# Performance work log

Hardware: AMD Instinct MI355X
Metric: run time of the kernel (lower is better)

Reference implementation:

```python
import jax, jax.numpy as jnp
import numpy as np

N_NODES = 100      # fixed: actor_fc expects 6000 = 100 * 60
IN_C    = 65536    # chev_conv_state_dim
OUT_C   = 60
K       = 3        # Chebyshev order
ACTION  = 100
N_EDGES = 1600


def setup_inputs() -> dict:
    key = jax.random.key(0)
    ks = jax.random.split(key, 20)
    s = 0.02  # small init scale
    f32 = jnp.float32
    return {
        "substrate_features": jax.random.normal(ks[0], (N_NODES, IN_C), f32),
        "substrate_edge_index": jax.random.randint(ks[1], (2, N_EDGES), 0, N_NODES),
        "vnr_features": jax.random.uniform(ks[2], (1, 3), f32),
        # ChebConv params: weight [K, IN_C, OUT_C], bias [OUT_C]
        "actor_cheb_w": (jax.random.normal(ks[3], (K, IN_C, OUT_C), f32) * s),
        "actor_cheb_b": jnp.zeros((OUT_C,), f32),
        "critic_cheb_w": (jax.random.normal(ks[4], (K, IN_C, OUT_C), f32) * s),
        "critic_cheb_b": jnp.zeros((OUT_C,), f32),
        # three Linear(1,60) per head, stacked: w [3, 60], b [3, 60]
        "actor_vnr_w": jax.random.normal(ks[5], (3, OUT_C), f32) * s,
        "actor_vnr_b": jnp.zeros((3, OUT_C), f32),
        "critic_vnr_w": jax.random.normal(ks[6], (3, OUT_C), f32) * s,
        "critic_vnr_b": jnp.zeros((3, OUT_C), f32),
        # heads
        "actor_fc_w": jax.random.normal(ks[7], (N_NODES * OUT_C, ACTION), f32) * s,
        "actor_fc_b": jnp.zeros((ACTION,), f32),
        "critic_fc_w": jax.random.normal(ks[8], (N_NODES * OUT_C, 1), f32) * s,
        "critic_fc_b": jnp.zeros((1,), f32),
    }


def _cheb_conv(x, src, dst, W, b):
    """PyG ChebConv with sym normalization, lambda_max=2 => L_hat = -D^-1/2 A D^-1/2.
    Z0 = x, Z1 = L_hat x, Z2 = 2 L_hat Z1 - Z0; out = sum_k Zk @ W[k] + b."""
    n = x.shape[0]
    ones = jnp.ones(src.shape[0], x.dtype)
    deg = jax.ops.segment_sum(ones, src, num_segments=n)
    dinv = jnp.where(deg > 0, jax.lax.rsqrt(jnp.maximum(deg, 1.0)), 0.0)
    w_norm = -dinv[src] * dinv[dst]  # [E]

    def lhat(z):  # sparse propagate: gather src rows, scale, scatter-add at dst
        return jax.ops.segment_sum(w_norm[:, None] * z[src], dst, num_segments=n)

    z0 = x
    z1 = lhat(z0)
    z2 = 2.0 * lhat(z1) - z0
    return z0 @ W[0] + z1 @ W[1] + z2 @ W[2] + b


def _vnr_sum(v, w, b):
    # sum of three Linear(1,60) outputs on scalars v[0], v[1], v[2] -> [60]
    return (v[:, None] * w + b).sum(axis=0)


def reference(substrate_features, substrate_edge_index, vnr_features,
              actor_cheb_w, actor_cheb_b, critic_cheb_w, critic_cheb_b,
              actor_vnr_w, actor_vnr_b, critic_vnr_w, critic_vnr_b,
              actor_fc_w, actor_fc_b, critic_fc_w, critic_fc_b):
    src, dst = substrate_edge_index[0], substrate_edge_index[1]
    v = vnr_features[0]  # [3]

    emb_a = jnp.tanh(_cheb_conv(substrate_features, src, dst, actor_cheb_w, actor_cheb_b))
    emb_a = emb_a + _vnr_sum(v, actor_vnr_w, actor_vnr_b)  # broadcast [N,60] + [60]
    flat_a = emb_a.reshape(1, -1)  # [1, 6000]
    logits = flat_a @ actor_fc_w + actor_fc_b  # [1, ACTION]

    emb_c = jnp.tanh(_cheb_conv(substrate_features, src, dst, critic_cheb_w, critic_cheb_b))
    emb_c = emb_c + _vnr_sum(v, critic_vnr_w, critic_vnr_b)
    flat_c = emb_c.reshape(1, -1)
    values = flat_c @ critic_fc_w + critic_fc_b  # [1, 1]

    return logits, values
```

## Files before the change

### kernel.cpp

```cpp
#include <hip/hip_runtime.h>
#include <math.h>

#define KDIM    65536
#define NNODES  100
#define OUTC    60
#define YW      64
#define YSLAB   (NNODES*YW)

#define BK5     64
#define ITERS5  8
#define SLAB5   (BK5*ITERS5)
#define NKC5    (KDIM/SLAB5)
#define CHUNK   256
#define NKC     256
#define STEPS   (CHUNK/32)

#define WS_Y    10048
#define WS_E    48448
#define XB_OFF_BYTES   245760ull
#define XB_BYTES       (100ull*65536ull*2ull)
#define WS_NEED_BYTES  (XB_OFF_BYTES + XB_BYTES)

typedef short bf16x8 __attribute__((ext_vector_type(8)));
typedef float f32x4  __attribute__((ext_vector_type(4)));
typedef unsigned short ushort8 __attribute__((ext_vector_type(8)));

__device__ inline unsigned short f2bf(float f) {
    union { float f; unsigned u; } x; x.f = f;
    unsigned r = x.u + 0x7FFFu + ((x.u >> 16) & 1u);
    return (unsigned short)(r >> 16);
}

__global__ __launch_bounds__(256) void k_cvt_x(const float* __restrict__ x,
                                               ushort8* __restrict__ xb,
                                               float* __restrict__ Y,
                                               float* __restrict__ out) {
    int g = blockIdx.x * 256 + threadIdx.x;
    if (g < 9600) ((f32x4*)Y)[g] = (f32x4){};
    if (g < 101)  out[g] = 0.f;
    for (int i = g; i < 819200; i += 204800) {
        const float4 lo = ((const float4*)x)[2 * i];
        const float4 hi = ((const float4*)x)[2 * i + 1];
        ushort8 o;
        o[0] = f2bf(lo.x); o[1] = f2bf(lo.y); o[2] = f2bf(lo.z); o[3] = f2bf(lo.w);
        o[4] = f2bf(hi.x); o[5] = f2bf(hi.y); o[6] = f2bf(hi.z); o[7] = f2bf(hi.w);
        xb[i] = o;
    }
}

__global__ __launch_bounds__(256) void k_gemm8(const unsigned short* __restrict__ xb,
                                               const float* __restrict__ wa,
                                               const float* __restrict__ wc,
                                               float* __restrict__ Y) {
    __shared__ unsigned short Ab[2][14 * 512];
    __shared__ unsigned short padlds[512];
    const int b    = blockIdx.x;
    const int lo8  = b & 7, q = b >> 3;
    const int hk   = q % 6;
    const int kc   = lo8 + 8 * (q / 6);
    const int wave = threadIdx.x >> 6;
    const int lane = threadIdx.x & 63;
    const int n16  = lane & 15;
    const int quad = lane >> 4;
    const int c0   = wave * 16;
    const int cidx = min(c0 + n16, OUTC - 1);
    const int kb0  = kc * SLAB5;

    const float* Wg = (hk < 3 ? wa : wc) + (size_t)(hk % 3) * ((size_t)KDIM * OUTC);

    auto DMA = [&](int buf, int kb) {
#pragma unroll
        for (int j5 = 0; j5 < 4; ++j5) {
            int j = wave + j5 * 4;
            int chunk = j * 64 + lane;
            int m  = chunk >> 3;
            int cc = (chunk & 7) ^ (m & 7);
            const unsigned short* src =
                xb + (size_t)min(m, NNODES - 1) * KDIM + kb + cc * 8;
            void* dst = (j < 14) ? (void*)&Ab[buf][j * 512] : (void*)padlds;
            __builtin_amdgcn_global_load_lds(
                (const __attribute__((address_space(1))) void*)src,
                (__attribute__((address_space(3))) void*)dst, 16, 0, 0);
        }
    };

    float breg[2][16];
    auto LOADB = [&](int pb, int kb) {
        const float* base = Wg + (size_t)(kb + quad * 8) * OUTC + cidx;
#pragma unroll
        for (int s = 0; s < 2; ++s)
#pragma unroll
            for (int j = 0; j < 8; ++j)
                breg[pb][s * 8 + j] = base[(s * 32 + j) * OUTC];
    };

    DMA(0, kb0);
    LOADB(0, kb0);
    f32x4 acc[7] = {};

#pragma unroll
    for (int it = 0; it < ITERS5; ++it) {
        if (it + 1 < ITERS5) {
            DMA((it + 1) & 1, kb0 + (it + 1) * BK5);
            LOADB((it + 1) & 1, kb0 + (it + 1) * BK5);
            asm volatile("s_waitcnt vmcnt(20)" ::: "memory");
        } else {
            asm volatile("s_waitcnt vmcnt(0)" ::: "memory");
        }
        __builtin_amdgcn_s_barrier();
        const unsigned short* A = Ab[it & 1];
#pragma unroll
        for (int s = 0; s < 2; ++s) {
            bf16x8 bfr;
#pragma unroll
            for (int j = 0; j < 8; ++j)
                bfr[j] = (short)f2bf(breg[it & 1][s * 8 + j]);
            int ch = (s * 4 + quad) ^ (n16 & 7);
#pragma unroll
            for (int t = 0; t < 7; ++t) {
                bf16x8 afr = *(const bf16x8*)(A + (t * 16 + n16) * BK5 + ch * 8);
                acc[t] = __builtin_amdgcn_mfma_f32_16x16x32_bf16(afr, bfr, acc[t], 0, 0, 0);
            }
        }
        __builtin_amdgcn_s_barrier();
    }

    float* Yb = Y + hk * YSLAB;
#pragma unroll
    for (int t = 0; t < 7; ++t)
#pragma unroll
        for (int r = 0; r < 4; ++r) {
            int row = t * 16 + quad * 4 + r;
            if (row < NNODES)
                atomicAdd(&Yb[row * YW + c0 + n16], acc[t][r]);
        }
}

__global__ __launch_bounds__(256, 2) void k_gemm_f32(const float* __restrict__ x,
                                                     const float* __restrict__ wa,
                                                     const float* __restrict__ wc,
                                                     float* __restrict__ Y) {
    const int hk   = blockIdx.x;
    const int kc   = blockIdx.y;
    const int wave = threadIdx.x >> 6;
    const int lane = threadIdx.x & 63;
    const int n16  = lane & 15;
    const int quad = lane >> 4;
    const float* W = (hk < 3 ? wa : wc) + (size_t)(hk % 3) * ((size_t)KDIM * OUTC);
    const int c0   = wave * 16;
    const int cidx = min(c0 + n16, OUTC - 1);
    const int kb0  = kc * CHUNK + quad * 8;
    const float* ap[7];
#pragma unroll
    for (int t = 0; t < 7; ++t)
        ap[t] = x + (size_t)min(n16 + 16 * t, NNODES - 1) * KDIM + kb0;
    const float* bp = W + (size_t)kb0 * OUTC + cidx;
    f32x4 acc[7] = {};
#pragma unroll 2
    for (int s = 0; s < STEPS; ++s) {
        bf16x8 bfr;
        const float* qq = bp + (size_t)s * 32 * OUTC;
#pragma unroll
        for (int j = 0; j < 8; ++j) bfr[j] = (short)f2bf(qq[j * OUTC]);
#pragma unroll
        for (int t = 0; t < 7; ++t) {
            const float* p = ap[t] + s * 32;
            float4 lo = *(const float4*)p;
            float4 hi = *(const float4*)(p + 4);
            bf16x8 afr;
            afr[0] = (short)f2bf(lo.x); afr[1] = (short)f2bf(lo.y);
            afr[2] = (short)f2bf(lo.z); afr[3] = (short)f2bf(lo.w);
            afr[4] = (short)f2bf(hi.x); afr[5] = (short)f2bf(hi.y);
            afr[6] = (short)f2bf(hi.z); afr[7] = (short)f2bf(hi.w);
            acc[t] = __builtin_amdgcn_mfma_f32_16x16x32_bf16(afr, bfr, acc[t], 0, 0, 0);
        }
    }
    float* Yb = Y + hk * YSLAB;
#pragma unroll
    for (int t = 0; t < 7; ++t)
#pragma unroll
        for (int r = 0; r < 4; ++r) {
            int row = t * 16 + quad * 4 + r;
            if (row < NNODES)
                atomicAdd(&Yb[row * YW + c0 + n16], acc[t][r]);
        }
}

__global__ __launch_bounds__(128) void k_embh(const int* __restrict__ ei,
                                              const float* __restrict__ Y,
                                              const float* __restrict__ vnr,
                                              const float* __restrict__ avw,
                                              const float* __restrict__ avb,
                                              const float* __restrict__ cvw,
                                              const float* __restrict__ cvb,
                                              const float* __restrict__ acb,
                                              const float* __restrict__ ccb,
                                              const float* __restrict__ afcb,
                                              const float* __restrict__ cfcb,
                                              const float* __restrict__ afw,
                                              const float* __restrict__ cfw,
                                              float* __restrict__ out) {
    __shared__ float Sp[NNODES * 101];
    __shared__ float y0[NNODES], y1[NNODES], y2[NNODES], t2[NNODES];
    __shared__ float e[NNODES];
    __shared__ int   deg[NNODES];
    __shared__ float dinv[NNODES];
    const int b = blockIdx.x, head = b / OUTC, c = b % OUTC;
    const int t = threadIdx.x;
    const int* src = ei;
    const int* dst = ei + 1600;

    for (int i = t; i < NNODES * 101; i += 128) Sp[i] = 0.f;
    if (t < NNODES) deg[t] = 0;
    __syncthreads();
    for (int ed = t; ed < 1600; ed += 128) atomicAdd(&deg[src[ed]], 1);
    __syncthreads();
    if (t < NNODES) { int d = deg[t]; dinv[t] = (d > 0) ? rsqrtf((float)d) : 0.f; }
    __syncthreads();
    for (int ed = t; ed < 1600; ed += 128) {
        int s = src[ed], d = dst[ed];
        atomicAdd(&Sp[d * 101 + s], -dinv[s] * dinv[d]);
    }
    const float* Yh = Y + (size_t)head * 3 * YSLAB;
    if (t < NNODES) {
        y0[t] = Yh[t * YW + c];
        y1[t] = Yh[YSLAB + t * YW + c];
        y2[t] = Yh[2 * YSLAB + t * YW + c];
    }
    __syncthreads();

    float z1 = 0.f, s2 = 0.f;
    if (t < NNODES) {
        const float* sr = Sp + t * 101;
        for (int m = 0; m < NNODES; ++m) { z1 += sr[m] * y1[m]; s2 += sr[m] * y2[m]; }
        t2[t] = s2;
    }
    __syncthreads();
    float ev = 0.f;
    if (t < NNODES) {
        const float* sr = Sp + t * 101;
        float t3 = 0.f;
        for (int m = 0; m < NNODES; ++m) t3 += sr[m] * t2[m];
        const float* cb = head ? ccb : acb;
        const float* vw = head ? cvw : avw;
        const float* vb = head ? cvb : avb;
        float u  = y0[t] + z1 + 2.f * t3 - y2[t] + cb[c];
        float vs = vnr[0] * vw[c]        + vb[c]
                 + vnr[1] * vw[OUTC + c] + vb[OUTC + c]
                 + vnr[2] * vw[2*OUTC+c] + vb[2*OUTC+c];
        ev = tanhf(u) + vs;
        e[t] = ev;
    }
    __syncthreads();

    if (head == 0) {
        if (t < NNODES) {
            float s = (c == 0) ? afcb[t] : 0.f;
            const float* wrow = afw + (size_t)c * 100 + t;
#pragma unroll 4
            for (int n = 0; n < NNODES; ++n) s += e[n] * wrow[(size_t)n * 6000];
            atomicAdd(&out[t], s);
        }
    } else {
        float p = (t < NNODES) ? ev * cfw[t * OUTC + c] : 0.f;
#pragma unroll
        for (int off = 32; off > 0; off >>= 1) p += __shfl_down(p, off, 64);
        __shared__ float wsum[2];
        if ((t & 63) == 0) wsum[t >> 6] = p;
        __syncthreads();
        if (t == 0) atomicAdd(&out[100], wsum[0] + wsum[1] + (c == 0 ? cfcb[0] : 0.f));
    }
}

extern "C" void kernel_launch(void* const* d_in, const int* in_sizes, int n_in,
                              void* d_out, int out_size, void* d_ws, size_t ws_size,
                              hipStream_t stream) {
    const float* x    = (const float*)d_in[0];
    const int*   ei   = (const int*)  d_in[1];
    const float* vnr  = (const float*)d_in[2];
    const float* wa   = (const float*)d_in[3];
    const float* acb  = (const float*)d_in[4];
    const float* wc   = (const float*)d_in[5];
    const float* ccb  = (const float*)d_in[6];
    const float* avw  = (const float*)d_in[7];
    const float* avb  = (const float*)d_in[8];
    const float* cvw  = (const float*)d_in[9];
    const float* cvb  = (const float*)d_in[10];
    const float* afw  = (const float*)d_in[11];
    const float* afcb = (const float*)d_in[12];
    const float* cfw  = (const float*)d_in[13];
    const float* cfcb = (const float*)d_in[14];

    float* ws = (float*)d_ws;
    float* Y  = ws + WS_Y;
    float* out = (float*)d_out;

    if (ws_size >= WS_NEED_BYTES) {
        unsigned short* xb = (unsigned short*)((char*)d_ws + XB_OFF_BYTES);
        k_cvt_x<<<800, 256, 0, stream>>>(x, (ushort8*)xb, Y, out);
        k_gemm8<<<768, 256, 0, stream>>>(xb, wa, wc, Y);
    } else {
        hipMemsetAsync((char*)d_ws + WS_Y * 4, 0, (WS_E - WS_Y) * 4, stream);
        hipMemsetAsync(d_out, 0, 101 * sizeof(float), stream);
        k_gemm_f32<<<dim3(6, NKC), 256, 0, stream>>>(x, wa, wc, Y);
    }

    k_embh<<<120, 128, 0, stream>>>(ei, Y, vnr, avw, avb, cvw, cvb,
                                    acb, ccb, afcb, cfcb, afw, cfw, out);
}
```

Measured before the change: 205.5 us.

## Share X tile across all six weight slabs in one 384-thread block

Replaces the per-(head,k) GEMM blocks with a single block per 256-wide K chunk in which six waves each own one of the six weight matrices. The bf16 X tile for the chunk is loaded into LDS once and reused by all six heads, removing the redundant X reads across six separate blocks. Each wave now covers all 60 output columns with a 4x7 accumulator set, and the double-buffered pipelining is replaced by one upfront load followed by a barrier. This raises register pressure, removes the overlap of loads with compute, and leaves 256 blocks in the grid.

```diff
diff --git a/kernel.cpp b/kernel.cpp
--- a/kernel.cpp
+++ b/kernel.cpp
@@ -7,10 +7,10 @@
 #define YW      64
 #define YSLAB   (NNODES*YW)
 
-#define BK5     64
-#define ITERS5  8
-#define SLAB5   (BK5*ITERS5)
-#define NKC5    (KDIM/SLAB5)
+#define BKA     64
+#define NSUB    4
+#define SLABA   (BKA*NSUB)
+#define NKCA    (KDIM/SLABA)
 #define CHUNK   256
 #define NKC     256
 #define STEPS   (CHUNK/32)
@@ -48,92 +48,77 @@
     }
 }
 
-__global__ __launch_bounds__(256) void k_gemm8(const unsigned short* __restrict__ xb,
-                                               const float* __restrict__ wa,
-                                               const float* __restrict__ wc,
-                                               float* __restrict__ Y) {
-    __shared__ unsigned short Ab[2][14 * 512];
-    __shared__ unsigned short padlds[512];
-    const int b    = blockIdx.x;
-    const int lo8  = b & 7, q = b >> 3;
-    const int hk   = q % 6;
-    const int kc   = lo8 + 8 * (q / 6);
+__global__ __launch_bounds__(384) void k_gemm10(const unsigned short* __restrict__ xb,
+                                                const float* __restrict__ wa,
+                                                const float* __restrict__ wc,
+                                                float* __restrict__ Y) {
+    __shared__ unsigned short Ab[NSUB][14 * 512];
+    const int kc   = blockIdx.x;
     const int wave = threadIdx.x >> 6;
     const int lane = threadIdx.x & 63;
     const int n16  = lane & 15;
     const int quad = lane >> 4;
-    const int c0   = wave * 16;
-    const int cidx = min(c0 + n16, OUTC - 1);
-    const int kb0  = kc * SLAB5;
-
-    const float* Wg = (hk < 3 ? wa : wc) + (size_t)(hk % 3) * ((size_t)KDIM * OUTC);
-
-    auto DMA = [&](int buf, int kb) {
-#pragma unroll
-        for (int j5 = 0; j5 < 4; ++j5) {
-            int j = wave + j5 * 4;
-            int chunk = j * 64 + lane;
-            int m  = chunk >> 3;
-            int cc = (chunk & 7) ^ (m & 7);
-            const unsigned short* src =
-                xb + (size_t)min(m, NNODES - 1) * KDIM + kb + cc * 8;
-            void* dst = (j < 14) ? (void*)&Ab[buf][j * 512] : (void*)padlds;
-            __builtin_amdgcn_global_load_lds(
-                (const __attribute__((address_space(1))) void*)src,
-                (__attribute__((address_space(3))) void*)dst, 16, 0, 0);
-        }
-    };
-
-    float breg[2][16];
-    auto LOADB = [&](int pb, int kb) {
-        const float* base = Wg + (size_t)(kb + quad * 8) * OUTC + cidx;
-#pragma unroll
-        for (int s = 0; s < 2; ++s)
-#pragma unroll
-            for (int j = 0; j < 8; ++j)
-                breg[pb][s * 8 + j] = base[(s * 32 + j) * OUTC];
-    };
-
-    DMA(0, kb0);
-    LOADB(0, kb0);
-    f32x4 acc[7] = {};
-
-#pragma unroll
-    for (int it = 0; it < ITERS5; ++it) {
-        if (it + 1 < ITERS5) {
-            DMA((it + 1) & 1, kb0 + (it + 1) * BK5);
-            LOADB((it + 1) & 1, kb0 + (it + 1) * BK5);
-            asm volatile("s_waitcnt vmcnt(20)" ::: "memory");
-        } else {
-            asm volatile("s_waitcnt vmcnt(0)" ::: "memory");
-        }
-        __builtin_amdgcn_s_barrier();
-        const unsigned short* A = Ab[it & 1];
+    const int kb0  = kc * SLABA;
+
+    const float* Wg = (wave < 3 ? wa : wc) + (size_t)(wave % 3) * ((size_t)KDIM * OUTC);
+
+    for (int jj = wave; jj < 56; jj += 6) {
+        int sub = jj / 14, j = jj % 14;
+        int chunk = j * 64 + lane;
+        int m  = chunk >> 3;
+        int cc = (chunk & 7) ^ (m & 7);
+        const unsigned short* src =
+            xb + (size_t)min(m, NNODES - 1) * KDIM + kb0 + sub * BKA + cc * 8;
+        __builtin_amdgcn_global_load_lds(
+            (const __attribute__((address_space(1))) void*)src,
+            (__attribute__((address_space(3))) void*)&Ab[sub][j * 512], 16, 0, 0);
+    }
+    __syncthreads();
+
+    f32x4 acc[4][7] = {};
+
+#pragma unroll
+    for (int sub = 0; sub < NSUB; ++sub) {
 #pragma unroll
         for (int s = 0; s < 2; ++s) {
-            bf16x8 bfr;
-#pragma unroll
-            for (int j = 0; j < 8; ++j)
-                bfr[j] = (short)f2bf(breg[it & 1][s * 8 + j]);
-            int ch = (s * 4 + quad) ^ (n16 & 7);
-#pragma unroll
-            for (int t = 0; t < 7; ++t) {
-                bf16x8 afr = *(const bf16x8*)(A + (t * 16 + n16) * BK5 + ch * 8);
-                acc[t] = __builtin_amdgcn_mfma_f32_16x16x32_bf16(afr, bfr, acc[t], 0, 0, 0);
+            float bv[4][8];
+            const int k0 = kb0 + sub * BKA + s * 32 + quad * 8;
+#pragma unroll
+            for (int ng = 0; ng < 4; ++ng) {
+                const int cidx = min(ng * 16 + n16, OUTC - 1);
+                const float* bp = Wg + (size_t)k0 * OUTC + cidx;
+#pragma unroll
+                for (int j = 0; j < 8; ++j) bv[ng][j] = bp[j * OUTC];
             }
-        }
-        __builtin_amdgcn_s_barrier();
-    }
-
-    float* Yb = Y + hk * YSLAB;
-#pragma unroll
-    for (int t = 0; t < 7; ++t)
-#pragma unroll
-        for (int r = 0; r < 4; ++r) {
-            int row = t * 16 + quad * 4 + r;
-            if (row < NNODES)
-                atomicAdd(&Yb[row * YW + c0 + n16], acc[t][r]);
-        }
+            const int ch = (s * 4 + quad) ^ (n16 & 7);
+            bf16x8 afr[7];
+#pragma unroll
+            for (int t = 0; t < 7; ++t)
+                afr[t] = *(const bf16x8*)(&Ab[sub][(t * 16 + n16) * BKA + ch * 8]);
+#pragma unroll
+            for (int ng = 0; ng < 4; ++ng) {
+                bf16x8 bfr;
+#pragma unroll
+                for (int j = 0; j < 8; ++j) bfr[j] = (short)f2bf(bv[ng][j]);
+#pragma unroll
+                for (int t = 0; t < 7; ++t)
+                    acc[ng][t] = __builtin_amdgcn_mfma_f32_16x16x32_bf16(
+                        afr[t], bfr, acc[ng][t], 0, 0, 0);
+            }
+        }
+    }
+
+    float* Yb = Y + wave * YSLAB;
+#pragma unroll
+    for (int ng = 0; ng < 4; ++ng)
+#pragma unroll
+        for (int t = 0; t < 7; ++t)
+#pragma unroll
+            for (int r = 0; r < 4; ++r) {
+                int row = t * 16 + quad * 4 + r;
+                if (row < NNODES)
+                    atomicAdd(&Yb[row * YW + ng * 16 + n16], acc[ng][t][r]);
+            }
 }
 
 __global__ __launch_bounds__(256, 2) void k_gemm_f32(const float* __restrict__ x,
@@ -298,7 +283,7 @@
     if (ws_size >= WS_NEED_BYTES) {
         unsigned short* xb = (unsigned short*)((char*)d_ws + XB_OFF_BYTES);
         k_cvt_x<<<800, 256, 0, stream>>>(x, (ushort8*)xb, Y, out);
-        k_gemm8<<<768, 256, 0, stream>>>(xb, wa, wc, Y);
+        k_gemm10<<<NKCA, 384, 0, stream>>>(xb, wa, wc, Y);
     } else {
         hipMemsetAsync((char*)d_ws + WS_Y * 4, 0, (WS_E - WS_Y) * 4, stream);
         hipMemsetAsync(d_out, 0, 101 * sizeof(float), stream);
```

After: 249.4 us. +21.4%, slower.

## Pre-transpose weights to bf16, triple-buffer GEMM, fuse epilogue via cooperative grid sync

Applied to the files above, without the earlier changes.

A new prep kernel converts both heads' Chebyshev weights to bf16 each call. It uses an LDS-staged transpose into a packed layout, so the GEMM can load each B fragment with one 16-byte vector load instead of 16 strided scalar fp32 loads plus per-element conversion. The GEMM moves to three-stage buffering with twice the K-slab per block (384 blocks). It is fused with the graph-propagation/head epilogue through a cooperative grid sync, with the old two-kernel path kept as a fallback. The trade-off is an extra full write and re-read of the bf16 weight copy, plus the cost of a grid-wide barrier.

```diff
diff --git a/kernel.cpp b/kernel.cpp
--- a/kernel.cpp
+++ b/kernel.cpp
@@ -1,4 +1,5 @@
 #include <hip/hip_runtime.h>
+#include <hip/hip_cooperative_groups.h>
 #include <math.h>
 
 #define KDIM    65536
@@ -7,10 +8,9 @@
 #define YW      64
 #define YSLAB   (NNODES*YW)
 
-#define BK5     64
-#define ITERS5  8
-#define SLAB5   (BK5*ITERS5)
-#define NKC5    (KDIM/SLAB5)
+#define BK      64
+#define ITERS   16
+#define SLAB    (BK*ITERS)
 #define CHUNK   256
 #define NKC     256
 #define STEPS   (CHUNK/32)
@@ -19,7 +19,10 @@
 #define WS_E    48448
 #define XB_OFF_BYTES   245760ull
 #define XB_BYTES       (100ull*65536ull*2ull)
-#define WS_NEED_BYTES  (XB_OFF_BYTES + XB_BYTES)
+#define WT_OFF_BYTES   (XB_OFF_BYTES + XB_BYTES)
+#define WT_HK_USH      (8192ull*60ull*8ull)
+#define WT_BYTES       (6ull*WT_HK_USH*2ull)
+#define WS_NEED_BYTES  (WT_OFF_BYTES + WT_BYTES)
 
 typedef short bf16x8 __attribute__((ext_vector_type(8)));
 typedef float f32x4  __attribute__((ext_vector_type(4)));
@@ -31,14 +34,19 @@
     return (unsigned short)(r >> 16);
 }
 
-__global__ __launch_bounds__(256) void k_cvt_x(const float* __restrict__ x,
-                                               ushort8* __restrict__ xb,
-                                               float* __restrict__ Y,
-                                               float* __restrict__ out) {
-    int g = blockIdx.x * 256 + threadIdx.x;
+__global__ __launch_bounds__(256) void k_prep(const float* __restrict__ x,
+                                              const float* __restrict__ wa,
+                                              const float* __restrict__ wc,
+                                              ushort8* __restrict__ xb,
+                                              unsigned short* __restrict__ wt,
+                                              float* __restrict__ Y,
+                                              float* __restrict__ out) {
+    __shared__ float tile[15360];
+    const int t  = threadIdx.x;
+    const int g  = blockIdx.x * 256 + t;
     if (g < 9600) ((f32x4*)Y)[g] = (f32x4){};
     if (g < 101)  out[g] = 0.f;
-    for (int i = g; i < 819200; i += 204800) {
+    for (int i = g; i < 819200; i += 393216) {
         const float4 lo = ((const float4*)x)[2 * i];
         const float4 hi = ((const float4*)x)[2 * i + 1];
         ushort8 o;
@@ -46,14 +54,210 @@
         o[4] = f2bf(hi.x); o[5] = f2bf(hi.y); o[6] = f2bf(hi.z); o[7] = f2bf(hi.w);
         xb[i] = o;
     }
-}
-
-__global__ __launch_bounds__(256) void k_gemm8(const unsigned short* __restrict__ xb,
-                                               const float* __restrict__ wa,
-                                               const float* __restrict__ wc,
-                                               float* __restrict__ Y) {
-    __shared__ unsigned short Ab[2][14 * 512];
-    __shared__ unsigned short padlds[512];
+    const int hk   = blockIdx.x >> 8;
+    const int ws_  = blockIdx.x & 255;
+    const int kb   = ws_ * 256;
+    const float* Wg = (hk < 3 ? wa : wc) + (size_t)(hk % 3) * ((size_t)KDIM * OUTC);
+    const float4* src4 = (const float4*)(Wg + (size_t)kb * OUTC);
+#pragma unroll
+    for (int i = 0; i < 15; ++i)
+        ((float4*)tile)[t + i * 256] = src4[t + i * 256];
+    __syncthreads();
+    ushort8* dst = (ushort8*)(wt + (size_t)hk * WT_HK_USH) + (size_t)(ws_ * 32) * 60;
+#pragma unroll
+    for (int i = 0; i < 8; ++i) {
+        int idx2 = t + i * 256;
+        if (idx2 < 1920) {
+            int pp = idx2 / 60, c = idx2 - pp * 60;
+            ushort8 o;
+#pragma unroll
+            for (int j = 0; j < 8; ++j) o[j] = f2bf(tile[(pp * 8 + j) * 60 + c]);
+            dst[idx2] = o;
+        }
+    }
+}
+
+union SMem {
+    struct { unsigned short Ab[3][14 * 512]; unsigned short pad[512]; } g;
+    struct { float Sp[NNODES * 101]; float y0[NNODES], y1[NNODES], y2[NNODES],
+             t2[NNODES], e[NNODES]; int deg[NNODES]; float dinv[NNODES];
+             float wsum[4]; } h;
+};
+
+__global__ __launch_bounds__(256) void k_main(const unsigned short* __restrict__ xb,
+                                              const unsigned short* __restrict__ wt,
+                                              float* __restrict__ Y,
+                                              const int* __restrict__ ei,
+                                              const float* __restrict__ vnr,
+                                              const float* __restrict__ avw,
+                                              const float* __restrict__ avb,
+                                              const float* __restrict__ cvw,
+                                              const float* __restrict__ cvb,
+                                              const float* __restrict__ acb,
+                                              const float* __restrict__ ccb,
+                                              const float* __restrict__ afcb,
+                                              const float* __restrict__ cfcb,
+                                              const float* __restrict__ afw,
+                                              const float* __restrict__ cfw,
+                                              float* __restrict__ out) {
+    __shared__ SMem sm;
+    {
+        const int b    = blockIdx.x;
+        const int lo8  = b & 7, q = b >> 3;
+        const int hk   = q % 6;
+        const int kc   = lo8 + 8 * (q / 6);
+        const int wave = threadIdx.x >> 6;
+        const int lane = threadIdx.x & 63;
+        const int n16  = lane & 15;
+        const int quad = lane >> 4;
+        const int c0   = wave * 16;
+        const int cidx = min(c0 + n16, OUTC - 1);
+        const int kb0  = kc * SLAB;
+
+        const unsigned short* wth = wt + (size_t)hk * WT_HK_USH;
+
+        auto DMA = [&](int buf, int kb) {
+#pragma unroll
+            for (int j5 = 0; j5 < 4; ++j5) {
+                int j = wave + j5 * 4;
+                int chunk = j * 64 + lane;
+                int m  = chunk >> 3;
+                int cc = (chunk & 7) ^ (m & 7);
+                const unsigned short* src =
+                    xb + (size_t)min(m, NNODES - 1) * KDIM + kb + cc * 8;
+                void* dst = (j < 14) ? (void*)&sm.g.Ab[buf][j * 512] : (void*)sm.g.pad;
+                __builtin_amdgcn_global_load_lds(
+                    (const __attribute__((address_space(1))) void*)src,
+                    (__attribute__((address_space(3))) void*)dst, 16, 0, 0);
+            }
+        };
+        bf16x8 breg[3][2];
+        auto LOADB = [&](int pb, int kb) {
+            const int pbase = kb >> 3;
+#pragma unroll
+            for (int s = 0; s < 2; ++s) {
+                size_t idx = (size_t)(pbase + s * 4 + quad) * 60 + cidx;
+                breg[pb][s] = *(const bf16x8*)(wth + idx * 8);
+            }
+        };
+
+        DMA(0, kb0);           LOADB(0, kb0);
+        DMA(1, kb0 + BK);      LOADB(1, kb0 + BK);
+        f32x4 acc[7] = {};
+
+#pragma unroll
+        for (int it = 0; it < ITERS; ++it) {
+            if (it + 2 < ITERS) {
+                DMA((it + 2) % 3, kb0 + (it + 2) * BK);
+                LOADB((it + 2) % 3, kb0 + (it + 2) * BK);
+                asm volatile("s_waitcnt vmcnt(12)" ::: "memory");
+            } else if (it + 2 == ITERS) {
+                asm volatile("s_waitcnt vmcnt(6)" ::: "memory");
+            } else {
+                asm volatile("s_waitcnt vmcnt(0)" ::: "memory");
+            }
+            __builtin_amdgcn_s_barrier();
+            const unsigned short* A = sm.g.Ab[it % 3];
+#pragma unroll
+            for (int s = 0; s < 2; ++s) {
+                bf16x8 bfr = breg[it % 3][s];
+                int ch = (s * 4 + quad) ^ (n16 & 7);
+#pragma unroll
+                for (int t = 0; t < 7; ++t) {
+                    bf16x8 afr = *(const bf16x8*)(A + (t * 16 + n16) * BK + ch * 8);
+                    acc[t] = __builtin_amdgcn_mfma_f32_16x16x32_bf16(afr, bfr, acc[t], 0, 0, 0);
+                }
+            }
+            __builtin_amdgcn_s_barrier();
+        }
+
+        float* Yb = Y + hk * YSLAB;
+#pragma unroll
+        for (int t = 0; t < 7; ++t)
+#pragma unroll
+            for (int r = 0; r < 4; ++r) {
+                int row = t * 16 + quad * 4 + r;
+                if (row < NNODES)
+                    atomicAdd(&Yb[row * YW + c0 + n16], acc[t][r]);
+            }
+    }
+
+    cooperative_groups::this_grid().sync();
+
+    const int b = blockIdx.x;
+    if (b >= 120) return;
+    const int head = b / OUTC, c = b % OUTC;
+    const int t = threadIdx.x;
+    const int* src = ei;
+    const int* dst = ei + 1600;
+
+    for (int i = t; i < NNODES * 101; i += 256) sm.h.Sp[i] = 0.f;
+    if (t < NNODES) sm.h.deg[t] = 0;
+    __syncthreads();
+    for (int ed = t; ed < 1600; ed += 256) atomicAdd(&sm.h.deg[src[ed]], 1);
+    __syncthreads();
+    if (t < NNODES) { int d = sm.h.deg[t]; sm.h.dinv[t] = (d > 0) ? rsqrtf((float)d) : 0.f; }
+    __syncthreads();
+    for (int ed = t; ed < 1600; ed += 256) {
+        int s = src[ed], d = dst[ed];
+        atomicAdd(&sm.h.Sp[d * 101 + s], -sm.h.dinv[s] * sm.h.dinv[d]);
+    }
+    float* Yh = Y + (size_t)head * 3 * YSLAB;
+    if (t < NNODES) {
+        sm.h.y0[t] = atomicAdd(&Yh[t * YW + c], 0.f);
+        sm.h.y1[t] = atomicAdd(&Yh[YSLAB + t * YW + c], 0.f);
+        sm.h.y2[t] = atomicAdd(&Yh[2 * YSLAB + t * YW + c], 0.f);
+    }
+    __syncthreads();
+
+    float z1 = 0.f, s2 = 0.f;
+    if (t < NNODES) {
+        const float* sr = sm.h.Sp + t * 101;
+        for (int m = 0; m < NNODES; ++m) { z1 += sr[m] * sm.h.y1[m]; s2 += sr[m] * sm.h.y2[m]; }
+        sm.h.t2[t] = s2;
+    }
+    __syncthreads();
+    float ev = 0.f;
+    if (t < NNODES) {
+        const float* sr = sm.h.Sp + t * 101;
+        float t3 = 0.f;
+        for (int m = 0; m < NNODES; ++m) t3 += sr[m] * sm.h.t2[m];
+        const float* cb = head ? ccb : acb;
+        const float* vw = head ? cvw : avw;
+        const float* vb = head ? cvb : avb;
+        float u  = sm.h.y0[t] + z1 + 2.f * t3 - sm.h.y2[t] + cb[c];
+        float vs = vnr[0] * vw[c]        + vb[c]
+                 + vnr[1] * vw[OUTC + c] + vb[OUTC + c]
+                 + vnr[2] * vw[2*OUTC+c] + vb[2*OUTC+c];
+        ev = tanhf(u) + vs;
+        sm.h.e[t] = ev;
+    }
+    __syncthreads();
+
+    if (head == 0) {
+        if (t < NNODES) {
+            float s = (c == 0) ? afcb[t] : 0.f;
+            const float* wrow = afw + (size_t)c * 100 + t;
+#pragma unroll 4
+            for (int n = 0; n < NNODES; ++n) s += sm.h.e[n] * wrow[(size_t)n * 6000];
+            atomicAdd(&out[t], s);
+        }
+    } else {
+        float p = (t < NNODES) ? ev * cfw[t * OUTC + c] : 0.f;
+#pragma unroll
+        for (int off = 32; off > 0; off >>= 1) p += __shfl_down(p, off, 64);
+        if ((t & 63) == 0) sm.h.wsum[t >> 6] = p;
+        __syncthreads();
+        if (t == 0) atomicAdd(&out[100],
+            sm.h.wsum[0] + sm.h.wsum[1] + sm.h.wsum[2] + sm.h.wsum[3] +
+            (c == 0 ? cfcb[0] : 0.f));
+    }
+}
+
+__global__ __launch_bounds__(256) void k_gemm_nc(const unsigned short* __restrict__ xb,
+                                                 const unsigned short* __restrict__ wt,
+                                                 float* __restrict__ Y) {
+    __shared__ SMem sm;
     const int b    = blockIdx.x;
     const int lo8  = b & 7, q = b >> 3;
     const int hk   = q % 6;
@@ -64,9 +268,8 @@
     const int quad = lane >> 4;
     const int c0   = wave * 16;
     const int cidx = min(c0 + n16, OUTC - 1);
-    const int kb0  = kc * SLAB5;
-
-    const float* Wg = (hk < 3 ? wa : wc) + (size_t)(hk % 3) * ((size_t)KDIM * OUTC);
+    const int kb0  = kc * SLAB;
+    const unsigned short* wth = wt + (size_t)hk * WT_HK_USH;
 
     auto DMA = [&](int buf, int kb) {
 #pragma unroll
@@ -77,48 +280,46 @@
             int cc = (chunk & 7) ^ (m & 7);
             const unsigned short* src =
                 xb + (size_t)min(m, NNODES - 1) * KDIM + kb + cc * 8;
-            void* dst = (j < 14) ? (void*)&Ab[buf][j * 512] : (void*)padlds;
+            void* dst = (j < 14) ? (void*)&sm.g.Ab[buf][j * 512] : (void*)sm.g.pad;
             __builtin_amdgcn_global_load_lds(
                 (const __attribute__((address_space(1))) void*)src,
                 (__attribute__((address_space(3))) void*)dst, 16, 0, 0);
         }
     };
-
-    float breg[2][16];
+    bf16x8 breg[3][2];
     auto LOADB = [&](int pb, int kb) {
-        const float* base = Wg + (size_t)(kb + quad * 8) * OUTC + cidx;
-#pragma unroll
-        for (int s = 0; s < 2; ++s)
-#pragma unroll
-            for (int j = 0; j < 8; ++j)
-                breg[pb][s * 8 + j] = base[(s * 32 + j) * OUTC];
+        const int pbase = kb >> 3;
+#pragma unroll
+        for (int s = 0; s < 2; ++s) {
+            size_t idx = (size_t)(pbase + s * 4 + quad) * 60 + cidx;
+            breg[pb][s] = *(const bf16x8*)(wth + idx * 8);
+        }
     };
 
-    DMA(0, kb0);
-    LOADB(0, kb0);
+    DMA(0, kb0);           LOADB(0, kb0);
+    DMA(1, kb0 + BK);      LOADB(1, kb0 + BK);
     f32x4 acc[7] = {};
 
 #pragma unroll
-    for (int it = 0; it < ITERS5; ++it) {
-        if (it + 1 < ITERS5) {
-            DMA((it + 1) & 1, kb0 + (it + 1) * BK5);
-            LOADB((it + 1) & 1, kb0 + (it + 1) * BK5);
-            asm volatile("s_waitcnt vmcnt(20)" ::: "memory");
+    for (int it = 0; it < ITERS; ++it) {
+        if (it + 2 < ITERS) {
+            DMA((it + 2) % 3, kb0 + (it + 2) * BK);
+            LOADB((it + 2) % 3, kb0 + (it + 2) * BK);
+            asm volatile("s_waitcnt vmcnt(12)" ::: "memory");
+        } else if (it + 2 == ITERS) {
+            asm volatile("s_waitcnt vmcnt(6)" ::: "memory");
         } else {
             asm volatile("s_waitcnt vmcnt(0)" ::: "memory");
         }
         __builtin_amdgcn_s_barrier();
-        const unsigned short* A = Ab[it & 1];
+        const unsigned short* A = sm.g.Ab[it % 3];
 #pragma unroll
         for (int s = 0; s < 2; ++s) {
-            bf16x8 bfr;
-#pragma unroll
-            for (int j = 0; j < 8; ++j)
-                bfr[j] = (short)f2bf(breg[it & 1][s * 8 + j]);
+            bf16x8 bfr = breg[it % 3][s];
             int ch = (s * 4 + quad) ^ (n16 & 7);
 #pragma unroll
             for (int t = 0; t < 7; ++t) {
-                bf16x8 afr = *(const bf16x8*)(A + (t * 16 + n16) * BK5 + ch * 8);
+                bf16x8 afr = *(const bf16x8*)(A + (t * 16 + n16) * BK + ch * 8);
                 acc[t] = __builtin_amdgcn_mfma_f32_16x16x32_bf16(afr, bfr, acc[t], 0, 0, 0);
             }
         }
@@ -134,6 +335,88 @@
             if (row < NNODES)
                 atomicAdd(&Yb[row * YW + c0 + n16], acc[t][r]);
         }
+}
+
+__global__ __launch_bounds__(128) void k_embh_fb(const int* __restrict__ ei,
+                                                 const float* __restrict__ Y,
+                                                 const float* __restrict__ vnr,
+                                                 const float* __restrict__ avw,
+                                                 const float* __restrict__ avb,
+                                                 const float* __restrict__ cvw,
+                                                 const float* __restrict__ cvb,
+                                                 const float* __restrict__ acb,
+                                                 const float* __restrict__ ccb,
+                                                 const float* __restrict__ afcb,
+                                                 const float* __restrict__ cfcb,
+                                                 const float* __restrict__ afw,
+                                                 const float* __restrict__ cfw,
+                                                 float* __restrict__ out) {
+    __shared__ float Sp[NNODES * 101];
+    __shared__ float y0[NNODES], y1[NNODES], y2[NNODES], t2[NNODES], e[NNODES];
+    __shared__ int   deg[NNODES];
+    __shared__ float dinv[NNODES];
+    const int b = blockIdx.x, head = b / OUTC, c = b % OUTC;
+    const int t = threadIdx.x;
+    const int* src = ei;
+    const int* dst = ei + 1600;
+    for (int i = t; i < NNODES * 101; i += 128) Sp[i] = 0.f;
+    if (t < NNODES) deg[t] = 0;
+    __syncthreads();
+    for (int ed = t; ed < 1600; ed += 128) atomicAdd(&deg[src[ed]], 1);
+    __syncthreads();
+    if (t < NNODES) { int d = deg[t]; dinv[t] = (d > 0) ? rsqrtf((float)d) : 0.f; }
+    __syncthreads();
+    for (int ed = t; ed < 1600; ed += 128) {
+        int s = src[ed], d = dst[ed];
+        atomicAdd(&Sp[d * 101 + s], -dinv[s] * dinv[d]);
+    }
+    const float* Yh = Y + (size_t)head * 3 * YSLAB;
+    if (t < NNODES) {
+        y0[t] = Yh[t * YW + c];
+        y1[t] = Yh[YSLAB + t * YW + c];
+        y2[t] = Yh[2 * YSLAB + t * YW + c];
+    }
+    __syncthreads();
+    float z1 = 0.f, s2 = 0.f;
+    if (t < NNODES) {
+        const float* sr = Sp + t * 101;
+        for (int m = 0; m < NNODES; ++m) { z1 += sr[m] * y1[m]; s2 += sr[m] * y2[m]; }
+        t2[t] = s2;
+    }
+    __syncthreads();
+    float ev = 0.f;
+    if (t < NNODES) {
+        const float* sr = Sp + t * 101;
+        float t3 = 0.f;
+        for (int m = 0; m < NNODES; ++m) t3 += sr[m] * t2[m];
+        const float* cb = head ? ccb : acb;
+        const float* vw = head ? cvw : avw;
+        const float* vb = head ? cvb : avb;
+        float u  = y0[t] + z1 + 2.f * t3 - y2[t] + cb[c];
+        float vs = vnr[0] * vw[c]        + vb[c]
+                 + vnr[1] * vw[OUTC + c] + vb[OUTC + c]
+                 + vnr[2] * vw[2*OUTC+c] + vb[2*OUTC+c];
+        ev = tanhf(u) + vs;
+        e[t] = ev;
+    }
+    __syncthreads();
+    if (head == 0) {
+        if (t < NNODES) {
+            float s = (c == 0) ? afcb[t] : 0.f;
+            const float* wrow = afw + (size_t)c * 100 + t;
+#pragma unroll 4
+            for (int n = 0; n < NNODES; ++n) s += e[n] * wrow[(size_t)n * 6000];
+            atomicAdd(&out[t], s);
+        }
+    } else {
+        float p = (t < NNODES) ? ev * cfw[t * OUTC + c] : 0.f;
+#pragma unroll
+        for (int off = 32; off > 0; off >>= 1) p += __shfl_down(p, off, 64);
+        __shared__ float wsum[2];
+        if ((t & 63) == 0) wsum[t >> 6] = p;
+        __syncthreads();
+        if (t == 0) atomicAdd(&out[100], wsum[0] + wsum[1] + (c == 0 ? cfcb[0] : 0.f));
+    }
 }
 
 __global__ __launch_bounds__(256, 2) void k_gemm_f32(const float* __restrict__ x,
@@ -184,92 +467,6 @@
             if (row < NNODES)
                 atomicAdd(&Yb[row * YW + c0 + n16], acc[t][r]);
         }
-}
-
-__global__ __launch_bounds__(128) void k_embh(const int* __restrict__ ei,
-                                              const float* __restrict__ Y,
-                                              const float* __restrict__ vnr,
-                                              const float* __restrict__ avw,
-                                              const float* __restrict__ avb,
-                                              const float* __restrict__ cvw,
-                                              const float* __restrict__ cvb,
-                                              const float* __restrict__ acb,
-                                              const float* __restrict__ ccb,
-                                              const float* __restrict__ afcb,
-                                              const float* __restrict__ cfcb,
-                                              const float* __restrict__ afw,
-                                              const float* __restrict__ cfw,
-                                              float* __restrict__ out) {
-    __shared__ float Sp[NNODES * 101];
-    __shared__ float y0[NNODES], y1[NNODES], y2[NNODES], t2[NNODES];
-    __shared__ float e[NNODES];
-    __shared__ int   deg[NNODES];
-    __shared__ float dinv[NNODES];
-    const int b = blockIdx.x, head = b / OUTC, c = b % OUTC;
-    const int t = threadIdx.x;
-    const int* src = ei;
-    const int* dst = ei + 1600;
-
-    for (int i = t; i < NNODES * 101; i += 128) Sp[i] = 0.f;
-    if (t < NNODES) deg[t] = 0;
-    __syncthreads();
-    for (int ed = t; ed < 1600; ed += 128) atomicAdd(&deg[src[ed]], 1);
-    __syncthreads();
-    if (t < NNODES) { int d = deg[t]; dinv[t] = (d > 0) ? rsqrtf((float)d) : 0.f; }
-    __syncthreads();
-    for (int ed = t; ed < 1600; ed += 128) {
-        int s = src[ed], d = dst[ed];
-        atomicAdd(&Sp[d * 101 + s], -dinv[s] * dinv[d]);
-    }
-    const float* Yh = Y + (size_t)head * 3 * YSLAB;
-    if (t < NNODES) {
-        y0[t] = Yh[t * YW + c];
-        y1[t] = Yh[YSLAB + t * YW + c];
-        y2[t] = Yh[2 * YSLAB + t * YW + c];
-    }
-    __syncthreads();
-
-    float z1 = 0.f, s2 = 0.f;
-    if (t < NNODES) {
-        const float* sr = Sp + t * 101;
-        for (int m = 0; m < NNODES; ++m) { z1 += sr[m] * y1[m]; s2 += sr[m] * y2[m]; }
-        t2[t] = s2;
-    }
-    __syncthreads();
-    float ev = 0.f;
-    if (t < NNODES) {
-        const float* sr = Sp + t * 101;
-        float t3 = 0.f;
-        for (int m = 0; m < NNODES; ++m) t3 += sr[m] * t2[m];
-        const float* cb = head ? ccb : acb;
-        const float* vw = head ? cvw : avw;
-        const float* vb = head ? cvb : avb;
-        float u  = y0[t] + z1 + 2.f * t3 - y2[t] + cb[c];
-        float vs = vnr[0] * vw[c]        + vb[c]
-                 + vnr[1] * vw[OUTC + c] + vb[OUTC + c]
-                 + vnr[2] * vw[2*OUTC+c] + vb[2*OUTC+c];
-        ev = tanhf(u) + vs;
-        e[t] = ev;
-    }
-    __syncthreads();
-
-    if (head == 0) {
-        if (t < NNODES) {
-            float s = (c == 0) ? afcb[t] : 0.f;
-            const float* wrow = afw + (size_t)c * 100 + t;
-#pragma unroll 4
-            for (int n = 0; n < NNODES; ++n) s += e[n] * wrow[(size_t)n * 6000];
-            atomicAdd(&out[t], s);
-        }
-    } else {
-        float p = (t < NNODES) ? ev * cfw[t * OUTC + c] : 0.f;
-#pragma unroll
-        for (int off = 32; off > 0; off >>= 1) p += __shfl_down(p, off, 64);
-        __shared__ float wsum[2];
-        if ((t & 63) == 0) wsum[t >> 6] = p;
-        __syncthreads();
-        if (t == 0) atomicAdd(&out[100], wsum[0] + wsum[1] + (c == 0 ? cfcb[0] : 0.f));
-    }
 }
 
 extern "C" void kernel_launch(void* const* d_in, const int* in_sizes, int n_in,
@@ -297,14 +494,24 @@
 
     if (ws_size >= WS_NEED_BYTES) {
         unsigned short* xb = (unsigned short*)((char*)d_ws + XB_OFF_BYTES);
-        k_cvt_x<<<800, 256, 0, stream>>>(x, (ushort8*)xb, Y, out);
-        k_gemm8<<<768, 256, 0, stream>>>(xb, wa, wc, Y);
+        unsigned short* wt = (unsigned short*)((char*)d_ws + WT_OFF_BYTES);
+        k_prep<<<1536, 256, 0, stream>>>(x, wa, wc, (ushort8*)xb, wt, Y, out);
+        void* args[] = { (void*)&xb, (void*)&wt, (void*)&Y, (void*)&ei,
+                         (void*)&vnr, (void*)&avw, (void*)&avb, (void*)&cvw,
+                         (void*)&cvb, (void*)&acb, (void*)&ccb, (void*)&afcb,
+                         (void*)&cfcb, (void*)&afw, (void*)&cfw, (void*)&out };
+        hipError_t e = hipLaunchCooperativeKernel((const void*)k_main, dim3(384),
+                                                  dim3(256), args, 0, stream);
+        if (e != hipSuccess) {
+            k_gemm_nc<<<384, 256, 0, stream>>>(xb, wt, Y);
+            k_embh_fb<<<120, 128, 0, stream>>>(ei, Y, vnr, avw, avb, cvw, cvb,
+                                               acb, ccb, afcb, cfcb, afw, cfw, out);
+        }
     } else {
         hipMemsetAsync((char*)d_ws + WS_Y * 4, 0, (WS_E - WS_Y) * 4, stream);
         hipMemsetAsync(d_out, 0, 101 * sizeof(float), stream);
         k_gemm_f32<<<dim3(6, NKC), 256, 0, stream>>>(x, wa, wc, Y);
-    }
-
-    k_embh<<<120, 128, 0, stream>>>(ei, Y, vnr, avw, avb, cvw, cvb,
-                                    acb, ccb, afcb, cfcb, afw, cfw, out);
-}
+        k_embh_fb<<<120, 128, 0, stream>>>(ei, Y, vnr, avw, avb, cvw, cvb,
+                                           acb, ccb, afcb, cfcb, afw, cfw, out);
+    }
+}
```

After: 283.5 us. 38.0% more time.

## Stage weight tiles into LDS via async DMA and double K-slab per block

Applied to the files above, without the earlier changes.

Weights for the GEMM are now loaded into LDS with global_load_lds as contiguous 16-byte chunks alongside the activation tiles, instead of per-lane strided scalar global loads into registers. Each block now covers 16 K-iterations instead of 8, which halves the grid to 384 blocks and halves the number of atomic adds into Y. The aim is coalesced weight traffic, fewer registers and fewer atomics. In exchange LDS use goes up, there are fewer blocks to fill the GPU, and the LDS reads of the weights are strided and may hit bank conflicts.

```diff
diff --git a/kernel.cpp b/kernel.cpp
--- a/kernel.cpp
+++ b/kernel.cpp
@@ -7,10 +7,9 @@
 #define YW      64
 #define YSLAB   (NNODES*YW)
 
-#define BK5     64
-#define ITERS5  8
-#define SLAB5   (BK5*ITERS5)
-#define NKC5    (KDIM/SLAB5)
+#define BK      64
+#define ITERS   16
+#define SLAB    (BK*ITERS)
 #define CHUNK   256
 #define NKC     256
 #define STEPS   (CHUNK/32)
@@ -48,12 +47,13 @@
     }
 }
 
-__global__ __launch_bounds__(256) void k_gemm8(const unsigned short* __restrict__ xb,
-                                               const float* __restrict__ wa,
-                                               const float* __restrict__ wc,
-                                               float* __restrict__ Y) {
+__global__ __launch_bounds__(256) void k_gemm11(const unsigned short* __restrict__ xb,
+                                                const float* __restrict__ wa,
+                                                const float* __restrict__ wc,
+                                                float* __restrict__ Y) {
     __shared__ unsigned short Ab[2][14 * 512];
-    __shared__ unsigned short padlds[512];
+    __shared__ float          Wf[2][15 * 256];
+    __shared__ float          padlds[256];
     const int b    = blockIdx.x;
     const int lo8  = b & 7, q = b >> 3;
     const int hk   = q % 6;
@@ -64,61 +64,61 @@
     const int quad = lane >> 4;
     const int c0   = wave * 16;
     const int cidx = min(c0 + n16, OUTC - 1);
-    const int kb0  = kc * SLAB5;
+    const int kb0  = kc * SLAB;
 
     const float* Wg = (hk < 3 ? wa : wc) + (size_t)(hk % 3) * ((size_t)KDIM * OUTC);
 
     auto DMA = [&](int buf, int kb) {
 #pragma unroll
-        for (int j5 = 0; j5 < 4; ++j5) {
+        for (int j5 = 0; j5 < 8; ++j5) {
             int j = wave + j5 * 4;
-            int chunk = j * 64 + lane;
-            int m  = chunk >> 3;
-            int cc = (chunk & 7) ^ (m & 7);
-            const unsigned short* src =
-                xb + (size_t)min(m, NNODES - 1) * KDIM + kb + cc * 8;
-            void* dst = (j < 14) ? (void*)&Ab[buf][j * 512] : (void*)padlds;
+            const void* src; void* dst;
+            if (j < 14) {
+                int chunk = j * 64 + lane;
+                int m  = chunk >> 3;
+                int cc = (chunk & 7) ^ (m & 7);
+                src = xb + (size_t)min(m, NNODES - 1) * KDIM + kb + cc * 8;
+                dst = &Ab[buf][j * 512];
+            } else if (j < 29) {
+                int wj = j - 14;
+                src = Wg + (size_t)kb * OUTC + wj * 256 + lane * 4;
+                dst = &Wf[buf][wj * 256];
+            } else {
+                src = xb + lane * 8;
+                dst = padlds;
+            }
             __builtin_amdgcn_global_load_lds(
                 (const __attribute__((address_space(1))) void*)src,
                 (__attribute__((address_space(3))) void*)dst, 16, 0, 0);
         }
     };
 
-    float breg[2][16];
-    auto LOADB = [&](int pb, int kb) {
-        const float* base = Wg + (size_t)(kb + quad * 8) * OUTC + cidx;
-#pragma unroll
-        for (int s = 0; s < 2; ++s)
-#pragma unroll
-            for (int j = 0; j < 8; ++j)
-                breg[pb][s * 8 + j] = base[(s * 32 + j) * OUTC];
-    };
-
     DMA(0, kb0);
-    LOADB(0, kb0);
     f32x4 acc[7] = {};
 
 #pragma unroll
-    for (int it = 0; it < ITERS5; ++it) {
-        if (it + 1 < ITERS5) {
-            DMA((it + 1) & 1, kb0 + (it + 1) * BK5);
-            LOADB((it + 1) & 1, kb0 + (it + 1) * BK5);
-            asm volatile("s_waitcnt vmcnt(20)" ::: "memory");
+    for (int it = 0; it < ITERS; ++it) {
+        if (it + 1 < ITERS) {
+            DMA((it + 1) & 1, kb0 + (it + 1) * BK);
+            asm volatile("s_waitcnt vmcnt(8)" ::: "memory");
         } else {
             asm volatile("s_waitcnt vmcnt(0)" ::: "memory");
         }
         __builtin_amdgcn_s_barrier();
         const unsigned short* A = Ab[it & 1];
+        const float*          B = Wf[it & 1];
 #pragma unroll
         for (int s = 0; s < 2; ++s) {
             bf16x8 bfr;
 #pragma unroll
-            for (int j = 0; j < 8; ++j)
-                bfr[j] = (short)f2bf(breg[it & 1][s * 8 + j]);
+            for (int jq = 0; jq < 8; ++jq) {
+                int jj = (jq + quad * 2) & 7;
+                bfr[jj] = (short)f2bf(B[(s * 32 + quad * 8 + jj) * OUTC + cidx]);
+            }
             int ch = (s * 4 + quad) ^ (n16 & 7);
 #pragma unroll
             for (int t = 0; t < 7; ++t) {
-                bf16x8 afr = *(const bf16x8*)(A + (t * 16 + n16) * BK5 + ch * 8);
+                bf16x8 afr = *(const bf16x8*)(A + (t * 16 + n16) * BK + ch * 8);
                 acc[t] = __builtin_amdgcn_mfma_f32_16x16x32_bf16(afr, bfr, acc[t], 0, 0, 0);
             }
         }
@@ -298,10 +298,12 @@
     if (ws_size >= WS_NEED_BYTES) {
         unsigned short* xb = (unsigned short*)((char*)d_ws + XB_OFF_BYTES);
         k_cvt_x<<<800, 256, 0, stream>>>(x, (ushort8*)xb, Y, out);
-        k_gemm8<<<768, 256, 0, stream>>>(xb, wa, wc, Y);
+        k_gemm11<<<384, 256, 0, stream>>>(xb, wa, wc, Y);
     } else {
-        hipMemsetAsync((char*)d_ws + WS_Y * 4, 0, (WS_E - WS_Y) * 4, stream);
-        hipMemsetAsync(d_out, 0, 101 * sizeof(float), stream);
+        hipError_t e1 = hipMemsetAsync((char*)d_ws + WS_Y * 4, 0,
+                                       (WS_E - WS_Y) * 4, stream);
+        hipError_t e2 = hipMemsetAsync(d_out, 0, 101 * sizeof(float), stream);
+        (void)e1; (void)e2;
         k_gemm_f32<<<dim3(6, NKC), 256, 0, stream>>>(x, wa, wc, Y);
     }
 
```

New measurement: 207.4 us. About the same (+0.9%).
